# Optimization experiments

Measured on AMD Instinct MI355X. Metric: run time of the kernel, lower is better.

The kernel has to match this reference:

```python
import jax, jax.numpy as jnp
import numpy as np

N_META, M_SUB = 64, 1024          # n meta-nodes, m nodes per sub-graph
D_IN, D_HID, D_OUT = 128, 128, 64
NUM_LAYERS_EXTRA, K = 2, 3        # total DSGraphGLayers = NUM_LAYERS_EXTRA + 1
N_EDGES = 1048576                 # ~avg degree 16 over 65536 nodes


def setup_inputs() -> dict:
    key = jax.random.key(0)
    ks = jax.random.split(key, 8)
    N = N_META * M_SUB
    x = jax.random.normal(ks[0], (N_META, M_SUB, D_IN), jnp.float32)
    sub_adj = jax.random.randint(ks[1], (2, N_EDGES), 0, N, dtype=jnp.int32)
    # dense binary meta-graph adjacency (n, n)
    adj = (jax.random.uniform(ks[2], (N_META, N_META)) < 0.1).astype(jnp.float32)
    L = NUM_LAYERS_EXTRA + 1
    scale = 1.0 / np.sqrt(D_HID).astype(np.float32)
    gcn_W = jax.random.normal(ks[3], (L, K + 1, D_HID, D_HID), jnp.float32) * scale
    gcn_b = jnp.zeros((L, K + 1, D_HID), jnp.float32)
    lin_W1 = jax.random.normal(ks[4], (D_HID, D_HID), jnp.float32) * scale
    lin_b1 = jnp.zeros((D_HID,), jnp.float32)
    lin_W2 = jax.random.normal(ks[5], (D_HID, D_OUT), jnp.float32) * scale
    lin_b2 = jnp.zeros((D_OUT,), jnp.float32)
    return dict(x=x, sub_adj=sub_adj, adj=adj, gcn_W=gcn_W, gcn_b=gcn_b,
                lin_W1=lin_W1, lin_b1=lin_b1, lin_W2=lin_W2, lin_b2=lin_b2)


def _gcn_conv(x, src, dst, dinv, W, b, N):
    norm = dinv[src] * dinv[dst]                      # [E+N]
    msg = (x @ W)[src] * norm[:, None]                # [E+N, d_out]
    return jax.ops.segment_sum(msg, dst, num_segments=N) + b


def reference(x, sub_adj, adj, gcn_W, gcn_b, lin_W1, lin_b1, lin_W2, lin_b2):
    n, m, d = x.shape
    N = n * m
    loops = jnp.arange(N, dtype=sub_adj.dtype)
    src = jnp.concatenate([sub_adj[0], loops])
    dst = jnp.concatenate([sub_adj[1], loops])
    deg = jax.ops.segment_sum(jnp.ones(src.shape, x.dtype), dst, num_segments=N)
    dinv = jnp.where(deg > 0, jax.lax.rsqrt(deg), jnp.zeros_like(deg))
    # precompute_adj: cached_adj = [adj, adj^2, ..., adj^K]; powers >= 2 detached in source
    cached = [adj]
    A = adj
    for _ in range(K - 1):
        A = jax.lax.stop_gradient(A @ adj)
        cached.append(A)
    for li in range(gcn_W.shape[0]):
        xf = x.reshape(N, -1)
        out = _gcn_conv(xf, src, dst, dinv, gcn_W[li, 0], gcn_b[li, 0], N)
        for i, Ai in enumerate(cached):
            # meta-graph mixing: x_i[n,m,d] = sum_j A_i[n,j] * x[j,m,d]
            xi = jnp.einsum('nj,jmd->nmd', Ai, x).reshape(N, -1)
            out = out + _gcn_conv(xi, src, dst, dinv, gcn_W[li, i + 1], gcn_b[li, i + 1], N)
        x = jax.nn.relu(out.reshape(n, m, -1))
    h = x.reshape(N, -1)
    h = jax.nn.relu(h @ lin_W1 + lin_b1)
    h = h @ lin_W2 + lin_b2
    return h.reshape(n, m, -1)
```

## Files before the change

kernel.cpp:

```cpp
#include <hip/hip_runtime.h>

#define NMETA 64
#define MSUB 1024
#define NNODES 65536
#define D 128
#define DOUT 64
#define NEDGES 1048576
#define COLS 131072
#define BCAP 5120

typedef __attribute__((ext_vector_type(8))) short bf8_t;
typedef __attribute__((ext_vector_type(4))) float f4_t;

__device__ inline unsigned short bfr(float x) {
    unsigned u = __builtin_bit_cast(unsigned, x);
    u += 0x7fffu + ((u >> 16) & 1u);
    return (unsigned short)(u >> 16);
}
__device__ inline float b2f(unsigned short h) {
    return __builtin_bit_cast(float, (unsigned)h << 16);
}
__device__ inline void unpack8(uint4 u, float* f) {
    f[0] = __builtin_bit_cast(float, u.x << 16);
    f[1] = __builtin_bit_cast(float, u.x & 0xffff0000u);
    f[2] = __builtin_bit_cast(float, u.y << 16);
    f[3] = __builtin_bit_cast(float, u.y & 0xffff0000u);
    f[4] = __builtin_bit_cast(float, u.z << 16);
    f[5] = __builtin_bit_cast(float, u.z & 0xffff0000u);
    f[6] = __builtin_bit_cast(float, u.w << 16);
    f[7] = __builtin_bit_cast(float, u.w & 0xffff0000u);
}

__global__ void k_zero256(int* __restrict__ p) { p[threadIdx.x] = 0; }

__global__ __launch_bounds__(256) void k_bhist(const int* __restrict__ dst,
                                               int* __restrict__ bcnt,
                                               int* __restrict__ wgoff) {
    __shared__ int c[256];
    int t = threadIdx.x, w = blockIdx.x;
    c[t] = 0;
    __syncthreads();
    const int* dp = dst + w * 4096;
    for (int k = 0; k < 16; ++k) atomicAdd(&c[dp[k * 256 + t] >> 8], 1);
    __syncthreads();
    wgoff[w * 256 + t] = atomicAdd(&bcnt[t], c[t]);
}

__global__ __launch_bounds__(256) void k_bscan(const int* __restrict__ bcnt,
                                               int* __restrict__ bbase) {
    __shared__ int sh[256];
    int t = threadIdx.x;
    int v = bcnt[t];
    sh[t] = v;
    __syncthreads();
    for (int d = 1; d < 256; d <<= 1) {
        int x = (t >= d) ? sh[t - d] : 0;
        __syncthreads();
        sh[t] += x;
        __syncthreads();
    }
    bbase[t] = sh[t] - v;
    if (t == 255) bbase[256] = NEDGES;
}

__global__ __launch_bounds__(256) void k_bscatter(const int* __restrict__ src,
                                                  const int* __restrict__ dst,
                                                  const int* __restrict__ bbase,
                                                  const int* __restrict__ wgoff,
                                                  unsigned* __restrict__ tmp) {
    __shared__ int cur[256];
    __shared__ int base[256];
    int t = threadIdx.x, w = blockIdx.x;
    cur[t] = 0;
    base[t] = bbase[t] + wgoff[w * 256 + t];
    __syncthreads();
    const int* dp = dst + w * 4096;
    const int* sp = src + w * 4096;
    for (int k = 0; k < 16; ++k) {
        int d = dp[k * 256 + t], s = sp[k * 256 + t];
        int b = d >> 8;
        int lr = atomicAdd(&cur[b], 1);
        tmp[base[b] + lr] = ((unsigned)(d & 255) << 16) | (unsigned)s;
    }
}

__global__ __launch_bounds__(256) void k_bcsr(const unsigned* __restrict__ tmp,
                                              const int* __restrict__ bbase,
                                              int* __restrict__ offs,
                                              float* __restrict__ dinv,
                                              unsigned short* __restrict__ csr16) {
    __shared__ unsigned pairs[BCAP];
    __shared__ unsigned short image[BCAP];
    __shared__ int cnt[256], cur[256], sh[256];
    int t = threadIdx.x, b = blockIdx.x;
    int base = bbase[b], n = bbase[b + 1] - base;
    for (int i = t; i < n; i += 256) pairs[i] = tmp[base + i];
    cnt[t] = 0;
    __syncthreads();
    for (int i = t; i < n; i += 256) atomicAdd(&cnt[pairs[i] >> 16], 1);
    __syncthreads();
    int c = cnt[t];
    sh[t] = c;
    __syncthreads();
    for (int d = 1; d < 256; d <<= 1) {
        int x = (t >= d) ? sh[t - d] : 0;
        __syncthreads();
        sh[t] += x;
        __syncthreads();
    }
    int excl = sh[t] - c;
    cur[t] = excl;
    offs[b * 256 + t] = base + excl;
    dinv[b * 256 + t] = rsqrtf((float)(c + 1));
    if (b == 255 && t == 255) offs[65536] = NEDGES;
    __syncthreads();
    for (int i = t; i < n; i += 256) {
        unsigned p = pairs[i];
        int pos = atomicAdd(&cur[p >> 16], 1);
        image[pos] = (unsigned short)(p & 0xffffu);
    }
    __syncthreads();
    for (int i = t; i < n; i += 256) csr16[base + i] = image[i];
}

__global__ __launch_bounds__(256) void k_adjpow(const float* __restrict__ A,
                                                unsigned short* __restrict__ Ab) {
    __shared__ float As[4096];
    __shared__ float Bs[4096];
    int t = threadIdx.x;
    for (int q = 0; q < 16; ++q) As[t + 256 * q] = A[t + 256 * q];
    __syncthreads();
    for (int q = 0; q < 16; ++q) {
        int idx = t + 256 * q;
        int n = idx >> 6, j = idx & 63;
        Ab[idx] = bfr(As[idx]);
        float acc = 0.f;
        for (int k = 0; k < 64; ++k) acc += As[n * 64 + k] * As[k * 64 + j];
        Bs[idx] = acc;
        Ab[4096 + idx] = bfr(acc);
    }
    __syncthreads();
    for (int q = 0; q < 16; ++q) {
        int idx = t + 256 * q;
        int n = idx >> 6, j = idx & 63;
        float acc = 0.f;
        for (int k = 0; k < 64; ++k) acc += Bs[n * 64 + k] * As[k * 64 + j];
        Ab[8192 + idx] = bfr(acc);
    }
}

__global__ void k_cvt_x(const float4* __restrict__ x, ushort4* __restrict__ o) {
    int i = blockIdx.x * 256 + threadIdx.x;
    float4 v = x[i];
    ushort4 u;
    u.x = bfr(v.x); u.y = bfr(v.y); u.z = bfr(v.z); u.w = bfr(v.w);
    o[i] = u;
}

__global__ __launch_bounds__(256) void k_cvt_w(const float* __restrict__ gcnW,
                                               const float* __restrict__ W1,
                                               const float* __restrict__ W2,
                                               unsigned short* __restrict__ Wt) {
    int b = blockIdx.x, t = threadIdx.x;
    int m = b >> 6;
    int idx = (b & 63) * 256 + t;
    const float* src;
    int N = 128;
    if (m < 12)       src = gcnW + m * 16384;
    else if (m == 12) src = W1;
    else { src = W2; N = 64; if (idx >= 8192) return; }
    int n = idx >> 7, k = idx & 127;
    Wt[m * 16384 + idx] = bfr(src[k * N + n]);
}

#define CPAD 258
__global__ __launch_bounds__(256) void k_mixX(const unsigned short* __restrict__ X,
                                              const unsigned short* __restrict__ Ab,
                                              unsigned short* __restrict__ Xm) {
    __shared__ unsigned short Us[64 * CPAD];
    int t = threadIdx.x;
    long c0 = (long)blockIdx.x * 256;
    int wave = t >> 6, lane = t & 63;
    int l16 = lane & 15, kg = lane >> 4;
    {
        int col = (t & 63) * 4;
        for (int q = 0; q < 16; ++q) {
            int row = q * 4 + (t >> 6);
            *(ushort4*)&Us[row * CPAD + col] =
                *(const ushort4*)(X + (long)row * COLS + c0 + col);
        }
    }
    bf8_t a[3][2];
#pragma unroll
    for (int i = 0; i < 3; ++i)
#pragma unroll
        for (int kb = 0; kb < 2; ++kb)
            a[i][kb] = *(const bf8_t*)(Ab + i * 4096 + (wave * 16 + l16) * 64 +
                                       kb * 32 + kg * 8);
    __syncthreads();
    f4_t zero4 = {0.f, 0.f, 0.f, 0.f};
    for (int cs = 0; cs < 16; ++cs) {
        int cc = cs * 16 + l16;
        bf8_t b0, b1;
#pragma unroll
        for (int jj = 0; jj < 8; ++jj) {
            b0[jj] = (short)Us[(kg * 8 + jj) * CPAD + cc];
            b1[jj] = (short)Us[(32 + kg * 8 + jj) * CPAD + cc];
        }
        f4_t acc0 = zero4, acc1 = zero4, acc2 = zero4;
        acc0 = __builtin_amdgcn_mfma_f32_16x16x32_bf16(a[0][0], b0, acc0, 0, 0, 0);
        acc1 = __builtin_amdgcn_mfma_f32_16x16x32_bf16(a[1][0], b0, acc1, 0, 0, 0);
        acc2 = __builtin_amdgcn_mfma_f32_16x16x32_bf16(a[2][0], b0, acc2, 0, 0, 0);
        acc0 = __builtin_amdgcn_mfma_f32_16x16x32_bf16(a[0][1], b1, acc0, 0, 0, 0);
        acc1 = __builtin_amdgcn_mfma_f32_16x16x32_bf16(a[1][1], b1, acc1, 0, 0, 0);
        acc2 = __builtin_amdgcn_mfma_f32_16x16x32_bf16(a[2][1], b1, acc2, 0, 0, 0);
#pragma unroll
        for (int r = 0; r < 4; ++r) {
            long n = wave * 16 + kg * 4 + r;
            long o = n * COLS + c0 + cc;
            Xm[o]                        = bfr(acc0[r]);
            Xm[(long)NNODES * D + o]     = bfr(acc1[r]);
            Xm[(long)2 * NNODES * D + o] = bfr(acc2[r]);
        }
    }
}

__global__ __launch_bounds__(256) void k_mgemm(const unsigned short* __restrict__ X0,
                                               const unsigned short* __restrict__ Xm,
                                               const unsigned short* __restrict__ Wt4,
                                               unsigned short* __restrict__ Y) {
    int wave = threadIdx.x >> 6, lane = threadIdx.x & 63;
    int l16 = lane & 15, kg = lane >> 4;
    long row0 = (long)blockIdx.x * 128 + wave * 32;

    f4_t acc[2][8];
    f4_t zero4 = {0.f, 0.f, 0.f, 0.f};
#pragma unroll
    for (int mt = 0; mt < 2; ++mt)
#pragma unroll
        for (int nt = 0; nt < 8; ++nt) acc[mt][nt] = zero4;

#pragma unroll
    for (int z = 0; z < 4; ++z) {
        const unsigned short* Xz = (z == 0) ? X0 : Xm + (long)(z - 1) * NNODES * D;
        const unsigned short* xp = Xz + row0 * 128 + kg * 8;
        const unsigned short* wp = Wt4 + z * 16384 + (long)l16 * 128 + kg * 8;
#pragma unroll
        for (int kb = 0; kb < 4; ++kb) {
            bf8_t a0 = *(const bf8_t*)(xp + (long)l16 * 128 + kb * 32);
            bf8_t a1 = *(const bf8_t*)(xp + (long)(l16 + 16) * 128 + kb * 32);
#pragma unroll
            for (int nt = 0; nt < 8; ++nt) {
                bf8_t b = *(const bf8_t*)(wp + nt * 16 * 128 + kb * 32);
                acc[0][nt] = __builtin_amdgcn_mfma_f32_16x16x32_bf16(a0, b, acc[0][nt], 0, 0, 0);
                acc[1][nt] = __builtin_amdgcn_mfma_f32_16x16x32_bf16(a1, b, acc[1][nt], 0, 0, 0);
            }
        }
    }
#pragma unroll
    for (int mt = 0; mt < 2; ++mt)
#pragma unroll
        for (int nt = 0; nt < 8; ++nt)
#pragma unroll
            for (int r = 0; r < 4; ++r) {
                long row = row0 + mt * 16 + kg * 4 + r;
                int col = nt * 16 + l16;
                Y[row * 128 + col] = bfr(acc[mt][nt][r]);
            }
}

template <int NT, bool RELU, bool OUT_BF16>
__global__ __launch_bounds__(256) void k_mfma(const unsigned short* __restrict__ X,
                                              const unsigned short* __restrict__ Wt,
                                              const float* __restrict__ bias,
                                              void* __restrict__ Cout) {
    int wave = threadIdx.x >> 6, lane = threadIdx.x & 63;
    int l16 = lane & 15, kg = lane >> 4;
    long row0 = (long)blockIdx.x * 128 + wave * 32;
    const int NCOL = NT * 16;

    bf8_t a[2][4];
    const unsigned short* xp = X + row0 * 128 + kg * 8;
#pragma unroll
    for (int kb = 0; kb < 4; ++kb) {
        a[0][kb] = *(const bf8_t*)(xp + (long)l16 * 128 + kb * 32);
        a[1][kb] = *(const bf8_t*)(xp + (long)(l16 + 16) * 128 + kb * 32);
    }
    f4_t acc[2][NT];
    f4_t zero4 = {0.f, 0.f, 0.f, 0.f};
#pragma unroll
    for (int mt = 0; mt < 2; ++mt)
#pragma unroll
        for (int nt = 0; nt < NT; ++nt) acc[mt][nt] = zero4;

    const unsigned short* wp = Wt + (long)l16 * 128 + kg * 8;
#pragma unroll
    for (int kb = 0; kb < 4; ++kb)
#pragma unroll
        for (int nt = 0; nt < NT; ++nt) {
            bf8_t b = *(const bf8_t*)(wp + nt * 16 * 128 + kb * 32);
            acc[0][nt] = __builtin_amdgcn_mfma_f32_16x16x32_bf16(a[0][kb], b, acc[0][nt], 0, 0, 0);
            acc[1][nt] = __builtin_amdgcn_mfma_f32_16x16x32_bf16(a[1][kb], b, acc[1][nt], 0, 0, 0);
        }
#pragma unroll
    for (int mt = 0; mt < 2; ++mt)
#pragma unroll
        for (int nt = 0; nt < NT; ++nt)
#pragma unroll
            for (int r = 0; r < 4; ++r) {
                long row = row0 + mt * 16 + kg * 4 + r;
                int col = nt * 16 + l16;
                float v = acc[mt][nt][r] + bias[col];
                if (RELU) v = fmaxf(v, 0.f);
                long o = row * NCOL + col;
                if (OUT_BF16) ((unsigned short*)Cout)[o] = bfr(v);
                else          ((float*)Cout)[o] = v;
            }
}

__global__ __launch_bounds__(256) void k_prop(const unsigned short* __restrict__ Y,
                                              const int* __restrict__ offs,
                                              const unsigned short* __restrict__ csr,
                                              const float* __restrict__ dinv,
                                              const float* __restrict__ bias4,
                                              unsigned short* __restrict__ Xout) {
    int wid = threadIdx.x >> 6;
    int lane = threadIdx.x & 63;
    int q = lane >> 4;
    int l = lane & 15;
    int v = blockIdx.x * 4 + wid;
    const uint4* Y4 = (const uint4*)Y;
    int e0 = offs[v], e1 = offs[v + 1];
    float acc[8];
#pragma unroll
    for (int k = 0; k < 8; ++k) acc[k] = 0.f;

    int e = e0 + q;
    for (; e + 4 < e1; e += 8) {
        int u0 = csr[e], u1 = csr[e + 4];
        float d0 = dinv[u0], d1 = dinv[u1];
        uint4 y0 = Y4[(long)u0 * 16 + l];
        uint4 y1 = Y4[(long)u1 * 16 + l];
        float f0[8], f1[8];
        unpack8(y0, f0);
        unpack8(y1, f1);
#pragma unroll
        for (int k = 0; k < 8; ++k) acc[k] += d0 * f0[k] + d1 * f1[k];
    }
    if (e < e1) {
        int u = csr[e];
        float du = dinv[u];
        uint4 y = Y4[(long)u * 16 + l];
        float f[8];
        unpack8(y, f);
#pragma unroll
        for (int k = 0; k < 8; ++k) acc[k] += du * f[k];
    }
#pragma unroll
    for (int k = 0; k < 8; ++k) {
        acc[k] += __shfl_xor(acc[k], 32, 64);
        acc[k] += __shfl_xor(acc[k], 16, 64);
    }
    if (q == 0) {
        float dv = dinv[v];
        float dvv = dv * dv;
        uint4 s = Y4[(long)v * 16 + l];
        float sf[8];
        unpack8(s, sf);
        float bs[8];
#pragma unroll
        for (int k = 0; k < 8; ++k) bs[k] = 0.f;
#pragma unroll
        for (int p = 0; p < 4; ++p) {
            float4 blo = *(const float4*)(bias4 + p * 128 + l * 8);
            float4 bhi = *(const float4*)(bias4 + p * 128 + l * 8 + 4);
            bs[0] += blo.x; bs[1] += blo.y; bs[2] += blo.z; bs[3] += blo.w;
            bs[4] += bhi.x; bs[5] += bhi.y; bs[6] += bhi.z; bs[7] += bhi.w;
        }
        unsigned r[8];
#pragma unroll
        for (int k = 0; k < 8; ++k)
            r[k] = bfr(fmaxf(dv * acc[k] + dvv * sf[k] + bs[k], 0.f));
        uint4 pk;
        pk.x = (r[1] << 16) | r[0];
        pk.y = (r[3] << 16) | r[2];
        pk.z = (r[5] << 16) | r[4];
        pk.w = (r[7] << 16) | r[6];
        ((uint4*)Xout)[(long)v * 16 + l] = pk;
    }
}

extern "C" void kernel_launch(void* const* d_in, const int* in_sizes, int n_in,
                              void* d_out, int out_size, void* d_ws, size_t ws_size,
                              hipStream_t stream) {
    const float* x      = (const float*)d_in[0];
    const int*   subadj = (const int*)d_in[1];
    const float* adj    = (const float*)d_in[2];
    const float* gcn_W  = (const float*)d_in[3];
    const float* gcn_b  = (const float*)d_in[4];
    const float* lin_W1 = (const float*)d_in[5];
    const float* lin_b1 = (const float*)d_in[6];
    const float* lin_W2 = (const float*)d_in[7];
    const float* lin_b2 = (const float*)d_in[8];
    float* out = (float*)d_out;

    const int* e_src = subadj;
    const int* e_dst = subadj + NEDGES;

    char* w = (char*)d_ws;
    int*      bcnt  = (int*)w;      w += (size_t)256 * 4;
    int*      bbase = (int*)w;      w += (size_t)260 * 4;
    int*      wgoff = (int*)w;      w += (size_t)65536 * 4;
    int*      offs  = (int*)w;      w += (size_t)65540 * 4;
    float*    dinv  = (float*)w;    w += (size_t)65536 * 4;
    unsigned* tmp   = (unsigned*)w; w += (size_t)NEDGES * 4;
    unsigned short* csr16 = (unsigned short*)w; w += (size_t)NEDGES * 2;
    unsigned short* Ab  = (unsigned short*)w; w += (size_t)3 * 4096 * 2;
    unsigned short* Xbf = (unsigned short*)w; w += (size_t)NNODES * D * 2;
    unsigned short* Xm  = (unsigned short*)w; w += (size_t)3 * NNODES * D * 2;
    unsigned short* Ybf = (unsigned short*)w; w += (size_t)NNODES * D * 2;
    unsigned short* Wt  = (unsigned short*)w; w += (size_t)14 * 16384 * 2;
    unsigned short* Hbf = (unsigned short*)w; w += (size_t)NNODES * D * 2;

    k_zero256<<<1, 256, 0, stream>>>(bcnt);
    k_bhist<<<256, 256, 0, stream>>>(e_dst, bcnt, wgoff);
    k_bscan<<<1, 256, 0, stream>>>(bcnt, bbase);
    k_bscatter<<<256, 256, 0, stream>>>(e_src, e_dst, bbase, wgoff, tmp);
    k_bcsr<<<256, 256, 0, stream>>>(tmp, bbase, offs, dinv, csr16);
    k_adjpow<<<1, 256, 0, stream>>>(adj, Ab);
    k_cvt_x<<<NNODES * D / 4 / 256, 256, 0, stream>>>((const float4*)x, (ushort4*)Xbf);
    k_cvt_w<<<896, 256, 0, stream>>>(gcn_W, lin_W1, lin_W2, Wt);

    for (int li = 0; li < 3; ++li) {
        k_mixX<<<COLS / 256, 256, 0, stream>>>(Xbf, Ab, Xm);
        k_mgemm<<<NNODES / 128, 256, 0, stream>>>(Xbf, Xm, Wt + (size_t)li * 4 * 16384, Ybf);
        k_prop<<<NNODES / 4, 256, 0, stream>>>(Ybf, offs, csr16, dinv,
                                               gcn_b + (size_t)li * 512, Xbf);
    }
    k_mfma<8, true, true><<<NNODES / 128, 256, 0, stream>>>(
        Xbf, Wt + (size_t)12 * 16384, lin_b1, Hbf);
    k_mfma<4, false, false><<<NNODES / 128, 256, 0, stream>>>(
        Hbf, Wt + (size_t)13 * 16384, lin_b2, out);
}
```

Before: 525.6 us.

## Halve GEMM tiles, merge setup kernels, drop atomic histogram, pack prop math

Several changes land together. The GEMM and mix kernels now use tiles half as tall (64 rows or 128 columns per block), doubling the number of blocks so more of the GPU is occupied. The adjacency-power, x-convert and weight-convert kernels are merged into one launch, and the zero kernel plus global atomics in the bucket histogram are replaced by a per-workgroup histogram that a serial scan turns into offsets. The propagation kernel accumulates with packed float2 math to encourage packed FMA instructions. The cost is less register reuse of B fragments per block and a slower serial loop in the scan.

```diff
diff --git a/kernel.cpp b/kernel.cpp
--- a/kernel.cpp
+++ b/kernel.cpp
@@ -11,6 +11,7 @@
 
 typedef __attribute__((ext_vector_type(8))) short bf8_t;
 typedef __attribute__((ext_vector_type(4))) float f4_t;
+typedef __attribute__((ext_vector_type(2))) float f2_t;
 
 __device__ inline unsigned short bfr(float x) {
     unsigned u = __builtin_bit_cast(unsigned, x);
@@ -20,22 +21,15 @@
 __device__ inline float b2f(unsigned short h) {
     return __builtin_bit_cast(float, (unsigned)h << 16);
 }
-__device__ inline void unpack8(uint4 u, float* f) {
-    f[0] = __builtin_bit_cast(float, u.x << 16);
-    f[1] = __builtin_bit_cast(float, u.x & 0xffff0000u);
-    f[2] = __builtin_bit_cast(float, u.y << 16);
-    f[3] = __builtin_bit_cast(float, u.y & 0xffff0000u);
-    f[4] = __builtin_bit_cast(float, u.z << 16);
-    f[5] = __builtin_bit_cast(float, u.z & 0xffff0000u);
-    f[6] = __builtin_bit_cast(float, u.w << 16);
-    f[7] = __builtin_bit_cast(float, u.w & 0xffff0000u);
-}
-
-__global__ void k_zero256(int* __restrict__ p) { p[threadIdx.x] = 0; }
+__device__ inline f2_t up2(unsigned u) {
+    f2_t r;
+    r[0] = __builtin_bit_cast(float, u << 16);
+    r[1] = __builtin_bit_cast(float, u & 0xffff0000u);
+    return r;
+}
 
 __global__ __launch_bounds__(256) void k_bhist(const int* __restrict__ dst,
-                                               int* __restrict__ bcnt,
-                                               int* __restrict__ wgoff) {
+                                               int* __restrict__ whist) {
     __shared__ int c[256];
     int t = threadIdx.x, w = blockIdx.x;
     c[t] = 0;
@@ -43,15 +37,20 @@
     const int* dp = dst + w * 4096;
     for (int k = 0; k < 16; ++k) atomicAdd(&c[dp[k * 256 + t] >> 8], 1);
     __syncthreads();
-    wgoff[w * 256 + t] = atomicAdd(&bcnt[t], c[t]);
-}
-
-__global__ __launch_bounds__(256) void k_bscan(const int* __restrict__ bcnt,
+    whist[t * 256 + w] = c[t];
+}
+
+__global__ __launch_bounds__(256) void k_bscan(int* __restrict__ whist,
                                                int* __restrict__ bbase) {
     __shared__ int sh[256];
     int t = threadIdx.x;
-    int v = bcnt[t];
-    sh[t] = v;
+    int run = 0;
+    for (int w = 0; w < 256; ++w) {
+        int v = whist[t * 256 + w];
+        whist[t * 256 + w] = run;
+        run += v;
+    }
+    sh[t] = run;
     __syncthreads();
     for (int d = 1; d < 256; d <<= 1) {
         int x = (t >= d) ? sh[t - d] : 0;
@@ -59,20 +58,20 @@
         sh[t] += x;
         __syncthreads();
     }
-    bbase[t] = sh[t] - v;
+    bbase[t] = sh[t] - run;
     if (t == 255) bbase[256] = NEDGES;
 }
 
 __global__ __launch_bounds__(256) void k_bscatter(const int* __restrict__ src,
                                                   const int* __restrict__ dst,
                                                   const int* __restrict__ bbase,
-                                                  const int* __restrict__ wgoff,
+                                                  const int* __restrict__ whist,
                                                   unsigned* __restrict__ tmp) {
     __shared__ int cur[256];
     __shared__ int base[256];
     int t = threadIdx.x, w = blockIdx.x;
     cur[t] = 0;
-    base[t] = bbase[t] + wgoff[w * 256 + t];
+    base[t] = bbase[t] + whist[t * 256 + w];
     __syncthreads();
     const int* dp = dst + w * 4096;
     const int* sp = src + w * 4096;
@@ -123,72 +122,71 @@
     for (int i = t; i < n; i += 256) csr16[base + i] = image[i];
 }
 
-__global__ __launch_bounds__(256) void k_adjpow(const float* __restrict__ A,
-                                                unsigned short* __restrict__ Ab) {
-    __shared__ float As[4096];
-    __shared__ float Bs[4096];
-    int t = threadIdx.x;
-    for (int q = 0; q < 16; ++q) As[t + 256 * q] = A[t + 256 * q];
-    __syncthreads();
-    for (int q = 0; q < 16; ++q) {
-        int idx = t + 256 * q;
-        int n = idx >> 6, j = idx & 63;
-        Ab[idx] = bfr(As[idx]);
-        float acc = 0.f;
-        for (int k = 0; k < 64; ++k) acc += As[n * 64 + k] * As[k * 64 + j];
-        Bs[idx] = acc;
-        Ab[4096 + idx] = bfr(acc);
-    }
-    __syncthreads();
-    for (int q = 0; q < 16; ++q) {
-        int idx = t + 256 * q;
-        int n = idx >> 6, j = idx & 63;
-        float acc = 0.f;
-        for (int k = 0; k < 64; ++k) acc += Bs[n * 64 + k] * As[k * 64 + j];
-        Ab[8192 + idx] = bfr(acc);
-    }
-}
-
-__global__ void k_cvt_x(const float4* __restrict__ x, ushort4* __restrict__ o) {
-    int i = blockIdx.x * 256 + threadIdx.x;
-    float4 v = x[i];
-    ushort4 u;
-    u.x = bfr(v.x); u.y = bfr(v.y); u.z = bfr(v.z); u.w = bfr(v.w);
-    o[i] = u;
-}
-
-__global__ __launch_bounds__(256) void k_cvt_w(const float* __restrict__ gcnW,
+__global__ __launch_bounds__(256) void k_setup(const float* __restrict__ A,
+                                               unsigned short* __restrict__ Ab,
+                                               const float4* __restrict__ x,
+                                               ushort4* __restrict__ xo,
+                                               const float* __restrict__ gcnW,
                                                const float* __restrict__ W1,
                                                const float* __restrict__ W2,
                                                unsigned short* __restrict__ Wt) {
-    int b = blockIdx.x, t = threadIdx.x;
-    int m = b >> 6;
-    int idx = (b & 63) * 256 + t;
-    const float* src;
-    int N = 128;
-    if (m < 12)       src = gcnW + m * 16384;
-    else if (m == 12) src = W1;
-    else { src = W2; N = 64; if (idx >= 8192) return; }
-    int n = idx >> 7, k = idx & 127;
-    Wt[m * 16384 + idx] = bfr(src[k * N + n]);
-}
-
-#define CPAD 258
+    int blk = blockIdx.x, t = threadIdx.x;
+    if (blk == 0) {
+        __shared__ float As[4096];
+        __shared__ float Bs[4096];
+        for (int q = 0; q < 16; ++q) As[t + 256 * q] = A[t + 256 * q];
+        __syncthreads();
+        for (int q = 0; q < 16; ++q) {
+            int idx = t + 256 * q;
+            int n = idx >> 6, j = idx & 63;
+            Ab[idx] = bfr(As[idx]);
+            float acc = 0.f;
+            for (int k = 0; k < 64; ++k) acc += As[n * 64 + k] * As[k * 64 + j];
+            Bs[idx] = acc;
+            Ab[4096 + idx] = bfr(acc);
+        }
+        __syncthreads();
+        for (int q = 0; q < 16; ++q) {
+            int idx = t + 256 * q;
+            int n = idx >> 6, j = idx & 63;
+            float acc = 0.f;
+            for (int k = 0; k < 64; ++k) acc += Bs[n * 64 + k] * As[k * 64 + j];
+            Ab[8192 + idx] = bfr(acc);
+        }
+    } else if (blk <= 8192) {
+        int i = (blk - 1) * 256 + t;
+        float4 v = x[i];
+        ushort4 u;
+        u.x = bfr(v.x); u.y = bfr(v.y); u.z = bfr(v.z); u.w = bfr(v.w);
+        xo[i] = u;
+    } else {
+        int b2 = blk - 8193;
+        int m = b2 >> 6;
+        int idx = (b2 & 63) * 256 + t;
+        const float* src;
+        int N = 128;
+        if (m < 12)       src = gcnW + m * 16384;
+        else if (m == 12) src = W1;
+        else { src = W2; N = 64; if (idx >= 8192) return; }
+        int n = idx >> 7, k = idx & 127;
+        Wt[m * 16384 + idx] = bfr(src[k * N + n]);
+    }
+}
+
+#define CPAD 130
 __global__ __launch_bounds__(256) void k_mixX(const unsigned short* __restrict__ X,
                                               const unsigned short* __restrict__ Ab,
                                               unsigned short* __restrict__ Xm) {
     __shared__ unsigned short Us[64 * CPAD];
     int t = threadIdx.x;
-    long c0 = (long)blockIdx.x * 256;
+    long c0 = (long)blockIdx.x * 128;
     int wave = t >> 6, lane = t & 63;
     int l16 = lane & 15, kg = lane >> 4;
-    {
-        int col = (t & 63) * 4;
-        for (int q = 0; q < 16; ++q) {
-            int row = q * 4 + (t >> 6);
-            *(ushort4*)&Us[row * CPAD + col] =
-                *(const ushort4*)(X + (long)row * COLS + c0 + col);
-        }
+    for (int q = 0; q < 8; ++q) {
+        int row = q * 8 + (t >> 5);
+        int col = (t & 31) * 4;
+        *(ushort4*)&Us[row * CPAD + col] =
+            *(const ushort4*)(X + (long)row * COLS + c0 + col);
     }
     bf8_t a[3][2];
 #pragma unroll
@@ -199,7 +197,7 @@
                                        kb * 32 + kg * 8);
     __syncthreads();
     f4_t zero4 = {0.f, 0.f, 0.f, 0.f};
-    for (int cs = 0; cs < 16; ++cs) {
+    for (int cs = 0; cs < 8; ++cs) {
         int cc = cs * 16 + l16;
         bf8_t b0, b1;
 #pragma unroll
@@ -231,42 +229,36 @@
                                                unsigned short* __restrict__ Y) {
     int wave = threadIdx.x >> 6, lane = threadIdx.x & 63;
     int l16 = lane & 15, kg = lane >> 4;
-    long row0 = (long)blockIdx.x * 128 + wave * 32;
-
-    f4_t acc[2][8];
+    long row0 = (long)blockIdx.x * 64 + wave * 16;
+
+    f4_t acc[8];
     f4_t zero4 = {0.f, 0.f, 0.f, 0.f};
 #pragma unroll
-    for (int mt = 0; mt < 2; ++mt)
-#pragma unroll
-        for (int nt = 0; nt < 8; ++nt) acc[mt][nt] = zero4;
+    for (int nt = 0; nt < 8; ++nt) acc[nt] = zero4;
 
 #pragma unroll
     for (int z = 0; z < 4; ++z) {
         const unsigned short* Xz = (z == 0) ? X0 : Xm + (long)(z - 1) * NNODES * D;
-        const unsigned short* xp = Xz + row0 * 128 + kg * 8;
+        const unsigned short* xp = Xz + (row0 + l16) * 128 + kg * 8;
         const unsigned short* wp = Wt4 + z * 16384 + (long)l16 * 128 + kg * 8;
 #pragma unroll
         for (int kb = 0; kb < 4; ++kb) {
-            bf8_t a0 = *(const bf8_t*)(xp + (long)l16 * 128 + kb * 32);
-            bf8_t a1 = *(const bf8_t*)(xp + (long)(l16 + 16) * 128 + kb * 32);
+            bf8_t a0 = *(const bf8_t*)(xp + kb * 32);
 #pragma unroll
             for (int nt = 0; nt < 8; ++nt) {
                 bf8_t b = *(const bf8_t*)(wp + nt * 16 * 128 + kb * 32);
-                acc[0][nt] = __builtin_amdgcn_mfma_f32_16x16x32_bf16(a0, b, acc[0][nt], 0, 0, 0);
-                acc[1][nt] = __builtin_amdgcn_mfma_f32_16x16x32_bf16(a1, b, acc[1][nt], 0, 0, 0);
+                acc[nt] = __builtin_amdgcn_mfma_f32_16x16x32_bf16(a0, b, acc[nt], 0, 0, 0);
             }
         }
     }
 #pragma unroll
-    for (int mt = 0; mt < 2; ++mt)
-#pragma unroll
-        for (int nt = 0; nt < 8; ++nt)
-#pragma unroll
-            for (int r = 0; r < 4; ++r) {
-                long row = row0 + mt * 16 + kg * 4 + r;
-                int col = nt * 16 + l16;
-                Y[row * 128 + col] = bfr(acc[mt][nt][r]);
-            }
+    for (int nt = 0; nt < 8; ++nt)
+#pragma unroll
+        for (int r = 0; r < 4; ++r) {
+            long row = row0 + kg * 4 + r;
+            int col = nt * 16 + l16;
+            Y[row * 128 + col] = bfr(acc[nt][r]);
+        }
 }
 
 template <int NT, bool RELU, bool OUT_BF16>
@@ -276,22 +268,18 @@
                                               void* __restrict__ Cout) {
     int wave = threadIdx.x >> 6, lane = threadIdx.x & 63;
     int l16 = lane & 15, kg = lane >> 4;
-    long row0 = (long)blockIdx.x * 128 + wave * 32;
+    long row0 = (long)blockIdx.x * 64 + wave * 16;
     const int NCOL = NT * 16;
 
-    bf8_t a[2][4];
-    const unsigned short* xp = X + row0 * 128 + kg * 8;
-#pragma unroll
-    for (int kb = 0; kb < 4; ++kb) {
-        a[0][kb] = *(const bf8_t*)(xp + (long)l16 * 128 + kb * 32);
-        a[1][kb] = *(const bf8_t*)(xp + (long)(l16 + 16) * 128 + kb * 32);
-    }
-    f4_t acc[2][NT];
+    bf8_t a[4];
+    const unsigned short* xp = X + (row0 + l16) * 128 + kg * 8;
+#pragma unroll
+    for (int kb = 0; kb < 4; ++kb) a[kb] = *(const bf8_t*)(xp + kb * 32);
+
+    f4_t acc[NT];
     f4_t zero4 = {0.f, 0.f, 0.f, 0.f};
 #pragma unroll
-    for (int mt = 0; mt < 2; ++mt)
-#pragma unroll
-        for (int nt = 0; nt < NT; ++nt) acc[mt][nt] = zero4;
+    for (int nt = 0; nt < NT; ++nt) acc[nt] = zero4;
 
     const unsigned short* wp = Wt + (long)l16 * 128 + kg * 8;
 #pragma unroll
@@ -299,23 +287,20 @@
 #pragma unroll
         for (int nt = 0; nt < NT; ++nt) {
             bf8_t b = *(const bf8_t*)(wp + nt * 16 * 128 + kb * 32);
-            acc[0][nt] = __builtin_amdgcn_mfma_f32_16x16x32_bf16(a[0][kb], b, acc[0][nt], 0, 0, 0);
-            acc[1][nt] = __builtin_amdgcn_mfma_f32_16x16x32_bf16(a[1][kb], b, acc[1][nt], 0, 0, 0);
-        }
-#pragma unroll
-    for (int mt = 0; mt < 2; ++mt)
-#pragma unroll
-        for (int nt = 0; nt < NT; ++nt)
-#pragma unroll
-            for (int r = 0; r < 4; ++r) {
-                long row = row0 + mt * 16 + kg * 4 + r;
-                int col = nt * 16 + l16;
-                float v = acc[mt][nt][r] + bias[col];
-                if (RELU) v = fmaxf(v, 0.f);
-                long o = row * NCOL + col;
-                if (OUT_BF16) ((unsigned short*)Cout)[o] = bfr(v);
-                else          ((float*)Cout)[o] = v;
-            }
+            acc[nt] = __builtin_amdgcn_mfma_f32_16x16x32_bf16(a[kb], b, acc[nt], 0, 0, 0);
+        }
+#pragma unroll
+    for (int nt = 0; nt < NT; ++nt)
+#pragma unroll
+        for (int r = 0; r < 4; ++r) {
+            long row = row0 + kg * 4 + r;
+            int col = nt * 16 + l16;
+            float v = acc[nt][r] + bias[col];
+            if (RELU) v = fmaxf(v, 0.f);
+            long o = row * NCOL + col;
+            if (OUT_BF16) ((unsigned short*)Cout)[o] = bfr(v);
+            else          ((float*)Cout)[o] = v;
+        }
 }
 
 __global__ __launch_bounds__(256) void k_prop(const unsigned short* __restrict__ Y,
@@ -331,9 +316,9 @@
     int v = blockIdx.x * 4 + wid;
     const uint4* Y4 = (const uint4*)Y;
     int e0 = offs[v], e1 = offs[v + 1];
-    float acc[8];
-#pragma unroll
-    for (int k = 0; k < 8; ++k) acc[k] = 0.f;
+    f2_t acc2[4];
+#pragma unroll
+    for (int k = 0; k < 4; ++k) acc2[k] = (f2_t){0.f, 0.f};
 
     int e = e0 + q;
     for (; e + 4 < e1; e += 8) {
@@ -341,21 +326,25 @@
         float d0 = dinv[u0], d1 = dinv[u1];
         uint4 y0 = Y4[(long)u0 * 16 + l];
         uint4 y1 = Y4[(long)u1 * 16 + l];
-        float f0[8], f1[8];
-        unpack8(y0, f0);
-        unpack8(y1, f1);
-#pragma unroll
-        for (int k = 0; k < 8; ++k) acc[k] += d0 * f0[k] + d1 * f1[k];
+        f2_t dd0 = {d0, d0}, dd1 = {d1, d1};
+        acc2[0] += dd0 * up2(y0.x) + dd1 * up2(y1.x);
+        acc2[1] += dd0 * up2(y0.y) + dd1 * up2(y1.y);
+        acc2[2] += dd0 * up2(y0.z) + dd1 * up2(y1.z);
+        acc2[3] += dd0 * up2(y0.w) + dd1 * up2(y1.w);
     }
     if (e < e1) {
         int u = csr[e];
         float du = dinv[u];
         uint4 y = Y4[(long)u * 16 + l];
-        float f[8];
-        unpack8(y, f);
-#pragma unroll
-        for (int k = 0; k < 8; ++k) acc[k] += du * f[k];
-    }
+        f2_t dd = {du, du};
+        acc2[0] += dd * up2(y.x);
+        acc2[1] += dd * up2(y.y);
+        acc2[2] += dd * up2(y.z);
+        acc2[3] += dd * up2(y.w);
+    }
+    float acc[8];
+#pragma unroll
+    for (int k = 0; k < 4; ++k) { acc[2 * k] = acc2[k][0]; acc[2 * k + 1] = acc2[k][1]; }
 #pragma unroll
     for (int k = 0; k < 8; ++k) {
         acc[k] += __shfl_xor(acc[k], 32, 64);
@@ -365,8 +354,7 @@
         float dv = dinv[v];
         float dvv = dv * dv;
         uint4 s = Y4[(long)v * 16 + l];
-        float sf[8];
-        unpack8(s, sf);
+        f2_t s2[4] = {up2(s.x), up2(s.y), up2(s.z), up2(s.w)};
         float bs[8];
 #pragma unroll
         for (int k = 0; k < 8; ++k) bs[k] = 0.f;
@@ -379,8 +367,10 @@
         }
         unsigned r[8];
 #pragma unroll
-        for (int k = 0; k < 8; ++k)
-            r[k] = bfr(fmaxf(dv * acc[k] + dvv * sf[k] + bs[k], 0.f));
+        for (int k = 0; k < 8; ++k) {
+            float sf = s2[k / 2][k % 2];
+            r[k] = bfr(fmaxf(dv * acc[k] + dvv * sf + bs[k], 0.f));
+        }
         uint4 pk;
         pk.x = (r[1] << 16) | r[0];
         pk.y = (r[3] << 16) | r[2];
@@ -408,9 +398,8 @@
     const int* e_dst = subadj + NEDGES;
 
     char* w = (char*)d_ws;
-    int*      bcnt  = (int*)w;      w += (size_t)256 * 4;
+    int*      whist = (int*)w;      w += (size_t)65536 * 4;
     int*      bbase = (int*)w;      w += (size_t)260 * 4;
-    int*      wgoff = (int*)w;      w += (size_t)65536 * 4;
     int*      offs  = (int*)w;      w += (size_t)65540 * 4;
     float*    dinv  = (float*)w;    w += (size_t)65536 * 4;
     unsigned* tmp   = (unsigned*)w; w += (size_t)NEDGES * 4;
@@ -422,23 +411,21 @@
     unsigned short* Wt  = (unsigned short*)w; w += (size_t)14 * 16384 * 2;
     unsigned short* Hbf = (unsigned short*)w; w += (size_t)NNODES * D * 2;
 
-    k_zero256<<<1, 256, 0, stream>>>(bcnt);
-    k_bhist<<<256, 256, 0, stream>>>(e_dst, bcnt, wgoff);
-    k_bscan<<<1, 256, 0, stream>>>(bcnt, bbase);
-    k_bscatter<<<256, 256, 0, stream>>>(e_src, e_dst, bbase, wgoff, tmp);
+    k_bhist<<<256, 256, 0, stream>>>(e_dst, whist);
+    k_bscan<<<1, 256, 0, stream>>>(whist, bbase);
+    k_bscatter<<<256, 256, 0, stream>>>(e_src, e_dst, bbase, whist, tmp);
     k_bcsr<<<256, 256, 0, stream>>>(tmp, bbase, offs, dinv, csr16);
-    k_adjpow<<<1, 256, 0, stream>>>(adj, Ab);
-    k_cvt_x<<<NNODES * D / 4 / 256, 256, 0, stream>>>((const float4*)x, (ushort4*)Xbf);
-    k_cvt_w<<<896, 256, 0, stream>>>(gcn_W, lin_W1, lin_W2, Wt);
+    k_setup<<<9089, 256, 0, stream>>>(adj, Ab, (const float4*)x, (ushort4*)Xbf,
+                                      gcn_W, lin_W1, lin_W2, Wt);
 
     for (int li = 0; li < 3; ++li) {
-        k_mixX<<<COLS / 256, 256, 0, stream>>>(Xbf, Ab, Xm);
-        k_mgemm<<<NNODES / 128, 256, 0, stream>>>(Xbf, Xm, Wt + (size_t)li * 4 * 16384, Ybf);
+        k_mixX<<<COLS / 128, 256, 0, stream>>>(Xbf, Ab, Xm);
+        k_mgemm<<<NNODES / 64, 256, 0, stream>>>(Xbf, Xm, Wt + (size_t)li * 4 * 16384, Ybf);
         k_prop<<<NNODES / 4, 256, 0, stream>>>(Ybf, offs, csr16, dinv,
                                                gcn_b + (size_t)li * 512, Xbf);
     }
-    k_mfma<8, true, true><<<NNODES / 128, 256, 0, stream>>>(
+    k_mfma<8, true, true><<<NNODES / 64, 256, 0, stream>>>(
         Xbf, Wt + (size_t)12 * 16384, lin_b1, Hbf);
-    k_mfma<4, false, false><<<NNODES / 128, 256, 0, stream>>>(
+    k_mfma<4, false, false><<<NNODES / 64, 256, 0, stream>>>(
         Hbf, Wt + (size_t)13 * 16384, lin_b2, out);
 }
```

New measurement: 595.4 us. 13.3% more time.
